# Optimization experiments

Hardware: AMD Instinct MI355X
Metric: run time of the kernel (lower is better)

The kernel has to match this reference:

```python
import jax, jax.numpy as jnp
import numpy as np
from jax import lax

DEPTH, HEADS, DH, DIM, M, V, NUM_EMB, D_VQ = 6, 8, 64, 512, 256, 523, 512, 64


def _ln(x, g, b):
    mu = jnp.mean(x, -1, keepdims=True)
    var = jnp.var(x, -1, keepdims=True)
    return (x - mu) * lax.rsqrt(var + 1e-5) * g + b


def _softmax_kernel(data, proj, is_query):
    # FAVOR+ positive softmax features (performer-pytorch softmax_kernel)
    dn = data * (data.shape[-1] ** -0.25)
    dd = jnp.einsum('bhld,md->bhlm', dn, proj)
    diag = 0.5 * jnp.sum(dn * dn, axis=-1, keepdims=True)
    mx = jnp.max(dd, axis=-1, keepdims=True) if is_query else jnp.max(dd)
    return jnp.exp(dd - diag - lax.stop_gradient(mx)) * (proj.shape[0] ** -0.5) + 1e-4


def _causal_linear_attn(qp, kp, v):
    # out_t = qp_t . cumsum_t(kp v^T) / (qp_t . cumsum_t(kp))
    kc = jnp.cumsum(kp, axis=2)
    den = jnp.einsum('bhlm,bhlm->bhl', qp, kc)
    kv = jnp.cumsum(jnp.einsum('bhlm,bhld->bhlmd', kp, v), axis=2)
    return jnp.einsum('bhlm,bhlmd->bhld', qp, kv) / den[..., None]


def _vq_encode(_x, conv1_w, conv1_b, conv2_w, conv2_b, codebook):
    dn = ('NCDHW', 'OIDHW', 'NCDHW')
    h = lax.conv_general_dilated(_x, conv1_w, (2, 2, 2), [(1, 1)] * 3, dimension_numbers=dn)
    h = jax.nn.relu(h + conv1_b[None, :, None, None, None])
    h = lax.conv_general_dilated(h, conv2_w, (2, 2, 2), [(1, 1)] * 3, dimension_numbers=dn)
    h = h + conv2_b[None, :, None, None, None]                 # [N, D, 4,4,4]
    z = jnp.transpose(h, (0, 2, 3, 4, 1))                      # [N, 4,4,4, D]
    flat = z.reshape(-1, z.shape[-1])
    d2 = (jnp.sum(flat * flat, 1, keepdims=True)
          - 2.0 * flat @ codebook.T
          + jnp.sum(codebook * codebook, 1)[None, :])
    inds = jnp.argmin(d2, axis=1).astype(jnp.int32)
    return inds.reshape(z.shape[:4])                           # [N, 4,4,4]


def _performer_loss(seq, tok_emb, pos_emb, proj, ln1_g, ln1_b, wq, wk, wv, wo, bo,
                    ln2_g, ln2_b, ff1_w, ff1_b, ff2_w, ff2_b, lnf_g, lnf_b,
                    logits_w, logits_b):
    inp, tgt = seq[:, :-1], seq[:, 1:]
    b, L = inp.shape
    h = tok_emb[inp] + pos_emb[:L][None]
    split = lambda t: jnp.transpose(t.reshape(b, L, HEADS, DH), (0, 2, 1, 3))
    for l in range(DEPTH):
        x1 = _ln(h, ln1_g[l], ln1_b[l])
        q, k, v = split(x1 @ wq[l]), split(x1 @ wk[l]), split(x1 @ wv[l])
        qp = _softmax_kernel(q, proj[l], True)
        kp = _softmax_kernel(k, proj[l], False)
        o = _causal_linear_attn(qp, kp, v)
        o = jnp.transpose(o, (0, 2, 1, 3)).reshape(b, L, DIM)
        h = h + o @ wo[l] + bo[l]
        x2 = _ln(h, ln2_g[l], ln2_b[l])
        h = h + jax.nn.gelu(x2 @ ff1_w[l] + ff1_b[l]) @ ff2_w[l] + ff2_b[l]
    h = _ln(h, lnf_g, lnf_b)
    logits = h @ logits_w + logits_b
    lp = jax.nn.log_softmax(logits, axis=-1)
    nll = -jnp.take_along_axis(lp, tgt[..., None], axis=-1)[..., 0]
    return jnp.mean(nll)


def setup_inputs() -> dict:
    key = jax.random.key(0)
    ks = jax.random.split(key, 24)
    n = lambda k, sh, s=0.02: (jax.random.normal(k, sh) * s).astype(jnp.float32)
    bs = 16
    return {
        'x': jax.random.normal(ks[0], (bs, 1, 16, 16, 16), jnp.float32),
        'xn': jax.random.normal(ks[1], (bs, 1, 1, 16, 16, 16), jnp.float32),
        'i': jax.random.randint(ks[2], (bs, 3), 0, V, jnp.int32),
        # frozen VQ-VAE
        'conv1_w': n(ks[3], (32, 1, 4, 4, 4), 0.1), 'conv1_b': jnp.zeros((32,), jnp.float32),
        'conv2_w': n(ks[4], (D_VQ, 32, 4, 4, 4), 0.05), 'conv2_b': jnp.zeros((D_VQ,), jnp.float32),
        'codebook': jax.random.normal(ks[5], (NUM_EMB, D_VQ), jnp.float32),
        # FAVOR+ random-feature projections (non-trainable buffer)
        'proj': jax.random.normal(ks[6], (DEPTH, M, DH), jnp.float32),
        # performer params
        'tok_emb': n(ks[7], (V, DIM)), 'pos_emb': n(ks[8], (131, DIM)),
        'ln1_g': jnp.ones((DEPTH, DIM), jnp.float32), 'ln1_b': jnp.zeros((DEPTH, DIM), jnp.float32),
        'wq': n(ks[9], (DEPTH, DIM, DIM)), 'wk': n(ks[10], (DEPTH, DIM, DIM)),
        'wv': n(ks[11], (DEPTH, DIM, DIM)), 'wo': n(ks[12], (DEPTH, DIM, DIM)),
        'bo': jnp.zeros((DEPTH, DIM), jnp.float32),
        'ln2_g': jnp.ones((DEPTH, DIM), jnp.float32), 'ln2_b': jnp.zeros((DEPTH, DIM), jnp.float32),
        'ff1_w': n(ks[13], (DEPTH, DIM, 4 * DIM)), 'ff1_b': jnp.zeros((DEPTH, 4 * DIM), jnp.float32),
        'ff2_w': n(ks[14], (DEPTH, 4 * DIM, DIM)), 'ff2_b': jnp.zeros((DEPTH, DIM), jnp.float32),
        'lnf_g': jnp.ones((DIM,), jnp.float32), 'lnf_b': jnp.zeros((DIM,), jnp.float32),
        'logits_w': n(ks[15], (DIM, V)), 'logits_b': jnp.zeros((V,), jnp.float32),
    }


def reference(x, xn, i, conv1_w, conv1_b, conv2_w, conv2_b, codebook, proj,
              tok_emb, pos_emb, ln1_g, ln1_b, wq, wk, wv, wo, bo, ln2_g, ln2_b,
              ff1_w, ff1_b, ff2_w, ff2_b, lnf_g, lnf_b, logits_w, logits_b):
    bs = x.shape[0]
    _xn = xn.reshape((-1,) + xn.shape[2:])            # (b n) c x y z
    _x = jnp.concatenate([x, _xn], axis=0)
    inds = _vq_encode(_x, conv1_w, conv1_b, conv2_w, conv2_b, codebook)
    inds_i = inds[:bs].reshape(bs, -1)                # b (x y z)
    inds_r = inds[bs:].reshape(bs, -1)                # b (n x y z)
    seq = jnp.concatenate([i.astype(jnp.int32), inds_r, inds_i], axis=1)  # [b, 131]
    return _performer_loss(seq, tok_emb, pos_emb, proj, ln1_g, ln1_b, wq, wk, wv, wo,
                           bo, ln2_g, ln2_b, ff1_w, ff1_b, ff2_w, ff2_b,
                           lnf_g, lnf_b, logits_w, logits_b)
```

## Files before the change

kernel.cpp:

```cpp
#include <hip/hip_runtime.h>

#define SEQL 130
#define LSEQ 131
#define DIMM 512
#define NHEADS 8
#define MF 256
#define VSZ 523
#define NROWS (16*SEQL)
#define NBH (16*NHEADS)
#define NBHL (NBH*SEQL)
#define QSEG 1064960
#define WLAYER 3145728

typedef __attribute__((ext_vector_type(8))) short short8;
typedef __attribute__((ext_vector_type(8))) unsigned short us8;
typedef __attribute__((ext_vector_type(4))) unsigned short us4;
typedef __attribute__((ext_vector_type(4))) float f32x4;

__device__ __forceinline__ unsigned short f2bf(float f){
  unsigned int u = __float_as_uint(f);
  u += 0x7fffu + ((u>>16)&1u);
  return (unsigned short)(u>>16);
}
__device__ __forceinline__ float bf2f(unsigned short h){
  return __uint_as_float(((unsigned int)h)<<16);
}
__device__ __forceinline__ float gelu_f(float x){
  float x3 = x*x*x;
  return 0.5f*x*(1.f+tanhf(0.7978845608028654f*(x+0.044715f*x3)));
}
__device__ __forceinline__ unsigned enc_max(float f){
  unsigned u = __float_as_uint(f);
  return (u & 0x80000000u) ? ~u : (u | 0x80000000u);
}
__device__ __forceinline__ float dec_max(unsigned k){
  unsigned u = (k>>31) ? (k & 0x7fffffffu) : ~k;
  return __uint_as_float(u);
}
__device__ __forceinline__ void gload16(const void* g, void* lds){
  __builtin_amdgcn_global_load_lds(
      (const __attribute__((address_space(1))) void*)g,
      (__attribute__((address_space(3))) void*)lds, 16, 0, 0);
}
__device__ __forceinline__ float blk_sum(float v){
  #pragma unroll
  for(int off=32;off;off>>=1) v += __shfl_xor(v,off);
  __shared__ float tmp_s[4];
  int t=threadIdx.x;
  if((t&63)==0) tmp_s[t>>6]=v;
  __syncthreads();
  v = tmp_s[0]+tmp_s[1]+tmp_s[2]+tmp_s[3];
  __syncthreads();
  return v;
}
__device__ __forceinline__ float blk_max(float v){
  #pragma unroll
  for(int off=32;off;off>>=1) v = fmaxf(v,__shfl_xor(v,off));
  __shared__ float tmp_m[4];
  int t=threadIdx.x;
  if((t&63)==0) tmp_m[t>>6]=v;
  __syncthreads();
  v = fmaxf(fmaxf(tmp_m[0],tmp_m[1]),fmaxf(tmp_m[2],tmp_m[3]));
  __syncthreads();
  return v;
}
__device__ __forceinline__ int tok_at(const int* __restrict__ iarr,
    const int* __restrict__ inds, int b, int p){
  if(p<3)  return iarr[b*3+p];
  if(p<67) return inds[(16+b)*64 + (p-3)];
  return inds[b*64 + (p-67)];
}

__global__ __launch_bounds__(256) void conv1_k(const float* __restrict__ x,
    const float* __restrict__ xn, const float* __restrict__ w,
    const float* __restrict__ bias, float* __restrict__ out){
  int idx = blockIdx.x*256 + threadIdx.x;
  if(idx >= 32*32*8*8*8) return;
  int ow = idx & 7, oh = (idx>>3)&7, od = (idx>>6)&7, oc = (idx>>9)&31, n = idx>>14;
  const float* xp = (n<16) ? (x + n*4096) : (xn + (n-16)*4096);
  const float* wp = w + oc*64;
  float acc = bias[oc];
  #pragma unroll
  for(int kd=0;kd<4;kd++){ int id = od*2-1+kd; if((unsigned)id>=16u) continue;
    #pragma unroll
    for(int kh=0;kh<4;kh++){ int ih = oh*2-1+kh; if((unsigned)ih>=16u) continue;
      #pragma unroll
      for(int kw=0;kw<4;kw++){ int iw = ow*2-1+kw; if((unsigned)iw>=16u) continue;
        acc += xp[(id*16+ih)*16+iw]*wp[(kd*4+kh)*4+kw];
      }}}
  out[idx] = fmaxf(acc,0.f);
}

__global__ __launch_bounds__(256) void cvt8_k(const float* __restrict__ src,
    unsigned short* __restrict__ dst, int n8){
  int i = blockIdx.x*256 + threadIdx.x;
  if(i >= n8) return;
  const float* s = src + (size_t)i*8;
  us8 u;
  #pragma unroll
  for(int j=0;j<8;j++) u[j] = f2bf(s[j]);
  *(us8*)(dst + (size_t)i*8) = u;
}

__global__ __launch_bounds__(256) void im2col_k(const float* __restrict__ c1,
    unsigned short* __restrict__ icol){
  int tid = blockIdx.x*256 + threadIdx.x;
  size_t e0 = (size_t)tid*8;
  int r = (int)(e0 >> 11);
  int k0 = (int)(e0 & 2047);
  int n = r>>6, od = (r>>4)&3, oh = (r>>2)&3, ow = r&3;
  int ic = k0>>6, kd = (k0>>4)&3, kh0 = (k0>>2)&3;
  int id = od*2 - 1 + kd;
  us8 u = {};
  if((unsigned)id < 8u){
    const float* base = c1 + (size_t)(n*32+ic)*512 + id*64;
    #pragma unroll
    for(int j=0;j<8;j++){
      int kh = kh0 + (j>>2), kw = j&3;
      int ih = oh*2 - 1 + kh, iw = ow*2 - 1 + kw;
      float v = 0.f;
      if((unsigned)ih < 8u && (unsigned)iw < 8u) v = base[ih*8 + iw];
      u[j] = f2bf(v);
    }
  }
  *(us8*)(icol + e0) = u;
}

__global__ __launch_bounds__(256) void vq_k(const float* __restrict__ z,
    const float* __restrict__ cb, int* __restrict__ inds){
  int nf = blockIdx.x;
  __shared__ float zs[64];
  int t = threadIdx.x;
  if(t<64) zs[t] = z[(size_t)nf*64 + t];
  __syncthreads();
  float best = 3.0e38f; int bi = 0;
  for(int j=t; j<512; j+=256){
    const float* cr = cb + j*64;
    float dot=0.f, nn=0.f;
    #pragma unroll 8
    for(int d=0;d<64;d++){ float cv=cr[d]; dot += zs[d]*cv; nn += cv*cv; }
    float dist = nn - 2.f*dot;
    if(dist < best){ best=dist; bi=j; }
  }
  #pragma unroll
  for(int off=32;off;off>>=1){
    float ob = __shfl_down(best,off); int oi = __shfl_down(bi,off);
    if(ob<best || (ob==best && oi<bi)){ best=ob; bi=oi; }
  }
  __shared__ float rb[4]; __shared__ int ri[4];
  if((t&63)==0){ rb[t>>6]=best; ri[t>>6]=bi; }
  __syncthreads();
  if(t==0){
    for(int wv=1;wv<4;wv++){ if(rb[wv]<best || (rb[wv]==best && ri[wv]<bi)){ best=rb[wv]; bi=ri[wv]; } }
    inds[nf]=bi;
  }
}

__global__ __launch_bounds__(256) void embed_k(const int* __restrict__ iarr,
    const int* __restrict__ inds, const float* __restrict__ tok,
    const float* __restrict__ pos, float* __restrict__ h){
  int idx = blockIdx.x*256 + threadIdx.x;
  int c = idx & 511; int row = idx >> 9;
  int b = row/SEQL, l = row - b*SEQL;
  int tk = tok_at(iarr, inds, b, l);
  h[idx] = tok[tk*DIMM + c] + pos[l*DIMM + c];
}

__global__ __launch_bounds__(256) void ln_k(const float* __restrict__ in,
    const float* __restrict__ g, const float* __restrict__ bb,
    unsigned short* __restrict__ out){
  int w = threadIdx.x>>6, l = threadIdx.x&63;
  int row = blockIdx.x*4 + w;
  const float* xr = in + (size_t)row*DIMM + l*8;
  f32x4 v0 = *(const f32x4*)xr;
  f32x4 v1 = *(const f32x4*)(xr+4);
  float s = v0[0]+v0[1]+v0[2]+v0[3]+v1[0]+v1[1]+v1[2]+v1[3];
  float ss = v0[0]*v0[0]+v0[1]*v0[1]+v0[2]*v0[2]+v0[3]*v0[3]
           + v1[0]*v1[0]+v1[1]*v1[1]+v1[2]*v1[2]+v1[3]*v1[3];
  #pragma unroll
  for(int off=32;off;off>>=1){ s += __shfl_xor(s,off); ss += __shfl_xor(ss,off); }
  float mu = s*(1.f/512.f);
  float var = ss*(1.f/512.f) - mu*mu;
  float inv = rsqrtf(var + 1e-5f);
  const float* gp = g + l*8; const float* bp = bb + l*8;
  us8 u;
  #pragma unroll
  for(int j=0;j<4;j++){
    u[j]   = f2bf((v0[j]-mu)*inv*gp[j]   + bp[j]);
    u[4+j] = f2bf((v1[j]-mu)*inv*gp[4+j] + bp[4+j]);
  }
  *(us8*)(out + (size_t)row*DIMM + l*8) = u;
}

__global__ __launch_bounds__(256) void wprep_k(const float* __restrict__ wq,
    const float* __restrict__ wk, const float* __restrict__ wv,
    const float* __restrict__ wo, const float* __restrict__ ff1,
    const float* __restrict__ ff2, unsigned short* __restrict__ wall,
    unsigned int* __restrict__ gmaxbits){
  int bid0 = blockIdx.x;
  int t = threadIdx.x;
  if(bid0==0 && t<8) gmaxbits[t] = 0u;
  int lyr = bid0 / 3072;
  int bid = bid0 - lyr*3072;
  unsigned short* wl = wall + (size_t)lyr*WLAYER;
  const float* src; unsigned short* dst;
  int n0, k0, srcN, dstK;
  if(bid < 768){
    int nt = bid % 48, kt = bid / 48;
    n0 = nt*32; k0 = kt*32;
    int seg = n0 >> 9;
    src = (seg==0 ? wq : seg==1 ? wk : wv) + (size_t)lyr*262144;
    dst = wl; srcN = 512; dstK = 512;
  } else if(bid < 1024){
    int b2 = bid-768; int nt = b2 % 16, kt = b2 / 16;
    n0 = nt*32; k0 = kt*32; src = wo + (size_t)lyr*262144;
    dst = wl + 786432; srcN = 512; dstK = 512;
  } else if(bid < 2048){
    int b2 = bid-1024; int nt = b2 % 64, kt = b2 / 64;
    n0 = nt*32; k0 = kt*32; src = ff1 + (size_t)lyr*1048576;
    dst = wl + 1048576; srcN = 2048; dstK = 512;
  } else {
    int b2 = bid-2048; int nt = b2 % 16, kt = b2 / 16;
    n0 = nt*32; k0 = kt*32; src = ff2 + (size_t)lyr*1048576;
    dst = wl + 2097152; srcN = 512; dstK = 2048;
  }
  int srcCol0 = (bid < 768) ? (n0 & 0x1ff) : n0;
  __shared__ float tile[32][33];
  int c = t&31, r = t>>5;
  #pragma unroll
  for(int j=0;j<4;j++)
    tile[r+8*j][c] = src[(size_t)(k0+r+8*j)*srcN + srcCol0 + c];
  __syncthreads();
  #pragma unroll
  for(int j=0;j<4;j++){
    int n = n0 + r + 8*j;
    dst[(size_t)n*dstK + k0 + c] = f2bf(tile[c][r+8*j]);
  }
}

__global__ __launch_bounds__(256) void wconv_k(const float* __restrict__ W,
    unsigned short* __restrict__ dst, int K, int N){
  __shared__ float tile[32][33];
  int k0 = blockIdx.y*32, n0 = blockIdx.x*32;
  int t = threadIdx.x; int c = t&31, r = t>>5;
  #pragma unroll
  for(int j=0;j<4;j++){
    int n = n0+c;
    tile[r+8*j][c] = (n<N) ? W[(size_t)(k0+r+8*j)*N + n] : 0.f;
  }
  __syncthreads();
  #pragma unroll
  for(int j=0;j<4;j++){
    int n = n0 + r + 8*j;
    if(n<N) dst[(size_t)n*K + k0 + c] = f2bf(tile[c][r+8*j]);
  }
}

template<int MODE>
__global__ __launch_bounds__(256) void gemm64x128_k(const unsigned short* __restrict__ A,
    const unsigned short* __restrict__ Bt, const float* __restrict__ bias,
    unsigned short* __restrict__ Cb, int M, int N, int K){
  __shared__ __attribute__((aligned(16))) unsigned short As[2][4096];
  __shared__ __attribute__((aligned(16))) unsigned short Bs[2][8192];
  int t = threadIdx.x, w = t>>6, l = t&63;
  const int m0 = blockIdx.y*64, n0 = blockIdx.x*128;
  int wr = w>>1, wc = w&1;
  f32x4 acc[2][4] = {};
  auto stage = [&](unsigned short* Ad, unsigned short* Bd, int k0){
    #pragma unroll
    for(int i=0;i<2;i++){
      int c = w*2 + i;
      int r = c*8 + (l>>3);
      int gc = k0 + (((l&7) ^ (r&7))<<3);
      int ar = m0 + r; if(ar >= M) ar = 0;
      gload16(A + (size_t)ar*K + gc, Ad + c*512);
    }
    #pragma unroll
    for(int i=0;i<4;i++){
      int c = w*4 + i;
      int r = c*8 + (l>>3);
      int gc = k0 + (((l&7) ^ (r&7))<<3);
      gload16(Bt + (size_t)(n0+r)*K + gc, Bd + c*512);
    }
  };
  stage(As[0], Bs[0], 0);
  int NTk = K>>6, buf = 0;
  for(int kt=0; kt<NTk; kt++){
    __syncthreads();
    if(kt+1 < NTk) stage(As[buf^1], Bs[buf^1], (kt+1)*64);
    const unsigned short* Ab = &As[buf][0];
    const unsigned short* Bb = &Bs[buf][0];
    #pragma unroll
    for(int kk=0;kk<2;kk++){
      short8 af[2], bf[4];
      #pragma unroll
      for(int m=0;m<2;m++){
        int row = wr*32 + m*16 + (l&15);
        int slot = kk*4 + (l>>4);
        af[m] = *(const short8*)(Ab + row*64 + ((slot^(row&7))<<3));
      }
      #pragma unroll
      for(int n=0;n<4;n++){
        int col = wc*64 + n*16 + (l&15);
        int slot = kk*4 + (l>>4);
        bf[n] = *(const short8*)(Bb + col*64 + ((slot^(col&7))<<3));
      }
      #pragma unroll
      for(int m=0;m<2;m++)
        #pragma unroll
        for(int n=0;n<4;n++)
          acc[m][n] = __builtin_amdgcn_mfma_f32_16x16x32_bf16(af[m], bf[n], acc[m][n], 0, 0, 0);
    }
    buf ^= 1;
  }
  #pragma unroll
  for(int m=0;m<2;m++){
    #pragma unroll
    for(int n=0;n<4;n++){
      int col = n0 + wc*64 + n*16 + (l&15);
      #pragma unroll
      for(int i=0;i<4;i++){
        int row = m0 + wr*32 + m*16 + (l>>4)*4 + i;
        if(row < M){
          float v = acc[m][n][i];
          if(MODE==1){
            v *= (col < 1024) ? 0.35355339059327378f : 1.0f;
            int seg = col>>9, d0 = col&511;
            int hh = d0>>6, d = d0&63;
            int bb = row/SEQL, ll = row - bb*SEQL;
            Cb[(size_t)seg*QSEG + (((size_t)(bb*NHEADS+hh))*SEQL + ll)*64 + d] = f2bf(v);
          } else {
            v += bias[col];
            v = gelu_f(v);
            Cb[(size_t)row*N+col] = f2bf(v);
          }
        }
      }
    }
  }
}

__global__ __launch_bounds__(256) void mgemm_k(const unsigned short* __restrict__ A,
    const unsigned short* __restrict__ Bt, const float* __restrict__ bias,
    float* __restrict__ Cf, int M, int N, int K){
  __shared__ __attribute__((aligned(16))) unsigned short As[2][4096];
  __shared__ __attribute__((aligned(16))) unsigned short Bs[2][4096];
  int t = threadIdx.x;
  const int m0 = blockIdx.y*64, n0 = blockIdx.x*64;
  int w = t>>6, l = t&63;
  int wr = w>>1, wc = w&1;
  f32x4 acc[2][2] = {};
  auto stage = [&](unsigned short* Ad, unsigned short* Bd, int k0){
    #pragma unroll
    for(int i=0;i<2;i++){
      int c = w*2 + i;
      int r = c*8 + (l>>3);
      int gc = k0 + (((l&7) ^ (r&7))<<3);
      int ar = m0 + r; if(ar >= M) ar = 0;
      gload16(A + (size_t)ar*K + gc, Ad + c*512);
      int br = n0 + r; if(br >= N) br = 0;
      gload16(Bt + (size_t)br*K + gc, Bd + c*512);
    }
  };
  stage(As[0], Bs[0], 0);
  int NT = K>>6;
  int buf = 0;
  for(int kt=0; kt<NT; kt++){
    __syncthreads();
    if(kt+1 < NT) stage(As[buf^1], Bs[buf^1], (kt+1)*64);
    const unsigned short* Ab = &As[buf][0];
    const unsigned short* Bb = &Bs[buf][0];
    #pragma unroll
    for(int kk=0;kk<2;kk++){
      short8 af[2], bf[2];
      #pragma unroll
      for(int m=0;m<2;m++){
        int row = wr*32 + m*16 + (l&15);
        int slot = kk*4 + (l>>4);
        af[m] = *(const short8*)(Ab + row*64 + ((slot^(row&7))<<3));
      }
      #pragma unroll
      for(int n=0;n<2;n++){
        int col = wc*32 + n*16 + (l&15);
        int slot = kk*4 + (l>>4);
        bf[n] = *(const short8*)(Bb + col*64 + ((slot^(col&7))<<3));
      }
      #pragma unroll
      for(int m=0;m<2;m++)
        #pragma unroll
        for(int n=0;n<2;n++)
          acc[m][n] = __builtin_amdgcn_mfma_f32_16x16x32_bf16(af[m], bf[n], acc[m][n], 0, 0, 0);
    }
    buf ^= 1;
  }
  #pragma unroll
  for(int m=0;m<2;m++){
    #pragma unroll
    for(int n=0;n<2;n++){
      int col = n0 + wc*32 + n*16 + (l&15);
      #pragma unroll
      for(int i=0;i<4;i++){
        int row = m0 + wr*32 + m*16 + (l>>4)*4 + i;
        if(row < M && col < N){
          Cf[(size_t)row*N+col] = acc[m][n][i] + bias[col];
        }
      }
    }
  }
}

template<int ACC>
__global__ __launch_bounds__(256) void mgemm32_k(const unsigned short* __restrict__ A,
    const unsigned short* __restrict__ Bt, const float* __restrict__ bias,
    float* __restrict__ Cf, int N, int K){
  __shared__ __attribute__((aligned(16))) unsigned short As[2][2048];
  __shared__ __attribute__((aligned(16))) unsigned short Bs[2][4096];
  int t = threadIdx.x;
  const int m0 = blockIdx.y*32, n0 = blockIdx.x*64;
  int w = t>>6, l = t&63;
  int wm = w&1, wn2 = w>>1;
  f32x4 acc[2] = {};
  auto stage = [&](unsigned short* Ad, unsigned short* Bd, int k0){
    {
      int c = w;
      int r = c*8 + (l>>3);
      int gc = k0 + (((l&7) ^ (r&7))<<3);
      gload16(A + (size_t)(m0+r)*K + gc, Ad + c*512);
    }
    #pragma unroll
    for(int i=0;i<2;i++){
      int c = w*2 + i;
      int r = c*8 + (l>>3);
      int gc = k0 + (((l&7) ^ (r&7))<<3);
      gload16(Bt + (size_t)(n0+r)*K + gc, Bd + c*512);
    }
  };
  stage(As[0], Bs[0], 0);
  int NT = K>>6;
  int buf = 0;
  for(int kt=0; kt<NT; kt++){
    __syncthreads();
    if(kt+1 < NT) stage(As[buf^1], Bs[buf^1], (kt+1)*64);
    const unsigned short* Ab = &As[buf][0];
    const unsigned short* Bb = &Bs[buf][0];
    #pragma unroll
    for(int kk=0;kk<2;kk++){
      int arow = wm*16 + (l&15);
      int slot = kk*4 + (l>>4);
      short8 af = *(const short8*)(Ab + arow*64 + ((slot^(arow&7))<<3));
      #pragma unroll
      for(int n=0;n<2;n++){
        int col = (wn2*2+n)*16 + (l&15);
        short8 bf = *(const short8*)(Bb + col*64 + ((slot^(col&7))<<3));
        acc[n] = __builtin_amdgcn_mfma_f32_16x16x32_bf16(af, bf, acc[n], 0, 0, 0);
      }
    }
    buf ^= 1;
  }
  #pragma unroll
  for(int n=0;n<2;n++){
    int col = n0 + (wn2*2+n)*16 + (l&15);
    float bv = bias[col];
    #pragma unroll
    for(int i=0;i<4;i++){
      int row = m0 + wm*16 + (l>>4)*4 + i;
      if(ACC) Cf[(size_t)row*N+col] += acc[n][i] + bv;
      else    Cf[(size_t)row*N+col]  = acc[n][i] + bv;
    }
  }
}

__global__ __launch_bounds__(256) void featA_k(const unsigned short* __restrict__ qn,
    const unsigned short* __restrict__ kn, const unsigned short* __restrict__ projl,
    unsigned short* __restrict__ qp, unsigned int* __restrict__ gmaxbits){
  int z = blockIdx.y;
  const unsigned short* dn = z ? kn : qn;
  __shared__ __attribute__((aligned(16))) float uni[32*264];
  __shared__ __attribute__((aligned(16))) unsigned short dns[2048];
  unsigned short* ps = (unsigned short*)uni;
  int t = threadIdx.x;
  int w = t>>6, l = t&63;
  size_t R0 = (size_t)blockIdx.x*32;
  {
    int c = w; int r = c*8 + (l>>3);
    int gc = (((l&7) ^ (r&7))<<3);
    gload16(dn + (R0+r)*64 + gc, dns + c*512);
  }
  #pragma unroll
  for(int i=0;i<8;i++){
    int c = w*8 + i; int r = c*8 + (l>>3);
    int gc = (((l&7) ^ (r&7))<<3);
    gload16(projl + (size_t)r*64 + gc, ps + c*512);
  }
  __syncthreads();
  int rt = w&1, cb = (w>>1)*8;
  f32x4 acc[8] = {};
  #pragma unroll
  for(int kk=0;kk<2;kk++){
    int ar = rt*16 + (l&15);
    int slot = kk*4 + (l>>4);
    short8 a = *(const short8*)(dns + ar*64 + ((slot^(ar&7))<<3));
    #pragma unroll
    for(int ct=0;ct<8;ct++){
      int br = (cb+ct)*16 + (l&15);
      short8 b = *(const short8*)(ps + br*64 + ((slot^(br&7))<<3));
      acc[ct] = __builtin_amdgcn_mfma_f32_16x16x32_bf16(a, b, acc[ct], 0, 0, 0);
    }
  }
  __syncthreads();
  #pragma unroll
  for(int ct=0;ct<8;ct++){
    int col = (cb+ct)*16 + (l&15);
    #pragma unroll
    for(int i=0;i<4;i++){
      int row = rt*16 + (l>>4)*4 + i;
      uni[row*264 + col] = acc[ct][i];
    }
  }
  __syncthreads();
  int r = t>>3, sub = t&7;
  float* rowp = uni + r*264 + sub*32;
  f32x4 v[8];
  #pragma unroll
  for(int jj=0;jj<8;jj++) v[jj] = *(const f32x4*)(rowp + jj*4);
  float m = -3.0e38f;
  #pragma unroll
  for(int jj=0;jj<8;jj++)
    #pragma unroll
    for(int i=0;i<4;i++) m = fmaxf(m, v[jj][i]);
  m = fmaxf(m, __shfl_xor(m,1));
  m = fmaxf(m, __shfl_xor(m,2));
  m = fmaxf(m, __shfl_xor(m,4));
  if(z==0){
    us8 dvu = *(const us8*)(dns + r*64 + ((sub^(r&7))<<3));
    float s2 = 0.f;
    #pragma unroll
    for(int j=0;j<8;j++){ float xx = bf2f(dvu[j]); s2 += xx*xx; }
    s2 += __shfl_xor(s2,1); s2 += __shfl_xor(s2,2); s2 += __shfl_xor(s2,4);
    float ds = 0.5f*s2;
    unsigned short* op = qp + (R0+r)*256 + sub*32;
    #pragma unroll
    for(int jj=0;jj<8;jj++){
      us4 u4;
      #pragma unroll
      for(int i=0;i<4;i++) u4[i] = f2bf(expf(v[jj][i] - ds - m)*0.0625f + 1e-4f);
      *(us4*)(op + jj*4) = u4;
    }
  } else {
    float bm = m;
    bm = fmaxf(bm, __shfl_xor(bm,8));
    bm = fmaxf(bm, __shfl_xor(bm,16));
    bm = fmaxf(bm, __shfl_xor(bm,32));
    __shared__ float wm[4];
    if(l==0) wm[w] = bm;
    __syncthreads();
    if(t==0){
      float g = fmaxf(fmaxf(wm[0],wm[1]),fmaxf(wm[2],wm[3]));
      atomicMax(gmaxbits, enc_max(g));
    }
  }
}

__global__ __launch_bounds__(256) void featB_k(const unsigned short* __restrict__ kn,
    const unsigned short* __restrict__ projl, const unsigned int* __restrict__ gmaxbits,
    unsigned short* __restrict__ kp){
  __shared__ __attribute__((aligned(16))) float uni[32*264];
  __shared__ __attribute__((aligned(16))) unsigned short dns[2048];
  unsigned short* ps = (unsigned short*)uni;
  int t = threadIdx.x;
  int w = t>>6, l = t&63;
  size_t R0 = (size_t)blockIdx.x*32;
  {
    int c = w; int r = c*8 + (l>>3);
    int gc = (((l&7) ^ (r&7))<<3);
    gload16(kn + (R0+r)*64 + gc, dns + c*512);
  }
  #pragma unroll
  for(int i=0;i<8;i++){
    int c = w*8 + i; int r = c*8 + (l>>3);
    int gc = (((l&7) ^ (r&7))<<3);
    gload16(projl + (size_t)r*64 + gc, ps + c*512);
  }
  __syncthreads();
  int rt = w&1, cb = (w>>1)*8;
  f32x4 acc[8] = {};
  #pragma unroll
  for(int kk=0;kk<2;kk++){
    int ar = rt*16 + (l&15);
    int slot = kk*4 + (l>>4);
    short8 a = *(const short8*)(dns + ar*64 + ((slot^(ar&7))<<3));
    #pragma unroll
    for(int ct=0;ct<8;ct++){
      int br = (cb+ct)*16 + (l&15);
      short8 b = *(const short8*)(ps + br*64 + ((slot^(br&7))<<3));
      acc[ct] = __builtin_amdgcn_mfma_f32_16x16x32_bf16(a, b, acc[ct], 0, 0, 0);
    }
  }
  __syncthreads();
  #pragma unroll
  for(int ct=0;ct<8;ct++){
    int col = (cb+ct)*16 + (l&15);
    #pragma unroll
    for(int i=0;i<4;i++){
      int row = rt*16 + (l>>4)*4 + i;
      uni[row*264 + col] = acc[ct][i];
    }
  }
  __syncthreads();
  float g = dec_max(gmaxbits[0]);
  int r = t>>3, sub = t&7;
  us8 dvu = *(const us8*)(dns + r*64 + ((sub^(r&7))<<3));
  float s2 = 0.f;
  #pragma unroll
  for(int j=0;j<8;j++){ float xx = bf2f(dvu[j]); s2 += xx*xx; }
  s2 += __shfl_xor(s2,1); s2 += __shfl_xor(s2,2); s2 += __shfl_xor(s2,4);
  float ds = 0.5f*s2;
  float* rowp = uni + r*264 + sub*32;
  unsigned short* op = kp + (R0+r)*256 + sub*32;
  #pragma unroll
  for(int jj=0;jj<8;jj++){
    f32x4 v = *(const f32x4*)(rowp + jj*4);
    us4 u4;
    #pragma unroll
    for(int i=0;i<4;i++) u4[i] = f2bf(expf(v[i] - ds - g)*0.0625f + 1e-4f);
    *(us4*)(op + jj*4) = u4;
  }
}

__global__ __launch_bounds__(256) void attn_k(const unsigned short* __restrict__ qp,
    const unsigned short* __restrict__ kp, const unsigned short* __restrict__ vn,
    unsigned short* __restrict__ ob){
  int qt = blockIdx.x, bh = blockIdx.y;
  int b = bh>>3, hh = bh&7;
  __shared__ __attribute__((aligned(16))) unsigned short qs[8192];
  __shared__ __attribute__((aligned(16))) unsigned short ks[8192];
  __shared__ __attribute__((aligned(16))) unsigned short VTs[64*34];
  __shared__ __attribute__((aligned(16))) unsigned short Sb[32*36];
  __shared__ float dens[2][32];
  int t = threadIdx.x;
  int w = t>>6, l = t&63;
  int qh = w>>1, nc = w&1;
  #pragma unroll
  for(int i=0;i<4;i++){
    int c = w*4 + i; int r = (c<<1) + (l>>5); int sl = l&31;
    int gc = ((sl ^ (r&7))<<3);
    int gr = qt*32 + r; if(gr >= SEQL) gr = 0;
    gload16(qp + ((size_t)bh*SEQL + gr)*256 + gc, qs + c*512);
  }
  if(t<64) dens[t>>5][t&31] = 0.f;
  f32x4 oacc[2] = {};
  for(int kt=0; kt<=qt; kt++){
    __syncthreads();
    #pragma unroll
    for(int i=0;i<4;i++){
      int c = w*4 + i; int r = (c<<1) + (l>>5); int sl = l&31;
      int gc = ((sl ^ (r&7))<<3);
      int gk = kt*32 + r; if(gk >= SEQL) gk = 0;
      gload16(kp + ((size_t)bh*SEQL + gk)*256 + gc, ks + c*512);
    }
    {
      int rr = t>>3, od = (t&7)*8;
      int gk = kt*32 + rr;
      us8 uv = {};
      if(gk < SEQL) uv = *(const us8*)(vn + ((size_t)bh*SEQL + gk)*64 + od);
      #pragma unroll
      for(int j=0;j<8;j++) VTs[(od+j)*34 + rr] = uv[j];
    }
    __syncthreads();
    f32x4 sacc = {};
    #pragma unroll
    for(int kk=0;kk<8;kk++){
      int ar = qh*16 + (l&15); int slot = kk*4 + (l>>4);
      short8 a = *(const short8*)(qs + ar*256 + ((slot^(ar&7))<<3));
      int br = nc*16 + (l&15);
      short8 bb2 = *(const short8*)(ks + br*256 + ((slot^(br&7))<<3));
      sacc = __builtin_amdgcn_mfma_f32_16x16x32_bf16(a, bb2, sacc, 0, 0, 0);
    }
    int scol = nc*16 + (l&15);
    int gcol = kt*32 + scol;
    float dp[4];
    #pragma unroll
    for(int i=0;i<4;i++){
      int sr = qh*16 + (l>>4)*4 + i;
      int grw = qt*32 + sr;
      float v2 = sacc[i];
      if(gcol > grw) v2 = 0.f;
      Sb[sr*36 + scol] = f2bf(v2);
      dp[i] = v2;
    }
    #pragma unroll
    for(int off=1;off<16;off<<=1)
      #pragma unroll
      for(int i=0;i<4;i++) dp[i] += __shfl_xor(dp[i], off);
    if((l&15)==0){
      #pragma unroll
      for(int i=0;i<4;i++) dens[nc][qh*16 + (l>>4)*4 + i] += dp[i];
    }
    __syncthreads();
    short8 a2 = *(const short8*)(Sb + (qh*16 + (l&15))*36 + (l>>4)*8);
    #pragma unroll
    for(int n2=0;n2<2;n2++){
      int d = nc*32 + n2*16 + (l&15);
      short8 b2 = *(const short8*)(VTs + d*34 + (l>>4)*8);
      oacc[n2] = __builtin_amdgcn_mfma_f32_16x16x32_bf16(a2, b2, oacc[n2], 0, 0, 0);
    }
  }
  __syncthreads();
  #pragma unroll
  for(int n2=0;n2<2;n2++){
    int d = nc*32 + n2*16 + (l&15);
    #pragma unroll
    for(int i=0;i<4;i++){
      int rit = qh*16 + (l>>4)*4 + i;
      int gr = qt*32 + rit;
      if(gr < SEQL){
        float inv = 1.f/(dens[0][rit] + dens[1][rit]);
        ob[((size_t)(b*SEQL+gr))*DIMM + hh*64 + d] = f2bf(oacc[n2][i]*inv);
      }
    }
  }
}

__global__ __launch_bounds__(256) void loss_k(const float* __restrict__ logits,
    const int* __restrict__ iarr, const int* __restrict__ inds,
    float* __restrict__ rnll){
  int row = blockIdx.x; int t = threadIdx.x;
  const float* lr = logits + (size_t)row*VSZ;
  float m = -3.0e38f;
  for(int j=t;j<VSZ;j+=256) m = fmaxf(m, lr[j]);
  m = blk_max(m);
  float s = 0.f;
  for(int j=t;j<VSZ;j+=256) s += expf(lr[j]-m);
  s = blk_sum(s);
  if(t==0){
    int b = row/SEQL, l = row - b*SEQL;
    int tgt = tok_at(iarr, inds, b, l+1);
    rnll[row] = (m + logf(s)) - lr[tgt];
  }
}

__global__ __launch_bounds__(256) void fin_k(const float* __restrict__ rnll,
    float* __restrict__ out){
  int t = threadIdx.x;
  float s = 0.f;
  for(int i=t;i<NROWS;i+=256) s += rnll[i];
  s = blk_sum(s);
  if(t==0) out[0] = s/(float)NROWS;
}

extern "C" void kernel_launch(void* const* d_in, const int* in_sizes, int n_in,
                              void* d_out, int out_size, void* d_ws, size_t ws_size,
                              hipStream_t stream){
  (void)in_sizes; (void)n_in; (void)out_size; (void)ws_size;
  const float* x        = (const float*)d_in[0];
  const float* xn       = (const float*)d_in[1];
  const int*   iarr     = (const int*)  d_in[2];
  const float* conv1_w  = (const float*)d_in[3];
  const float* conv1_b  = (const float*)d_in[4];
  const float* conv2_w  = (const float*)d_in[5];
  const float* conv2_b  = (const float*)d_in[6];
  const float* codebook = (const float*)d_in[7];
  const float* proj     = (const float*)d_in[8];
  const float* tok_emb  = (const float*)d_in[9];
  const float* pos_emb  = (const float*)d_in[10];
  const float* ln1_g    = (const float*)d_in[11];
  const float* ln1_b    = (const float*)d_in[12];
  const float* wq       = (const float*)d_in[13];
  const float* wk       = (const float*)d_in[14];
  const float* wv       = (const float*)d_in[15];
  const float* wo       = (const float*)d_in[16];
  const float* bo       = (const float*)d_in[17];
  const float* ln2_g    = (const float*)d_in[18];
  const float* ln2_b    = (const float*)d_in[19];
  const float* ff1_w    = (const float*)d_in[20];
  const float* ff1_b    = (const float*)d_in[21];
  const float* ff2_w    = (const float*)d_in[22];
  const float* ff2_b    = (const float*)d_in[23];
  const float* lnf_g    = (const float*)d_in[24];
  const float* lnf_b    = (const float*)d_in[25];
  const float* logits_w = (const float*)d_in[26];
  const float* logits_b = (const float*)d_in[27];

  float* wsf = (float*)d_ws;
  size_t off = 0;
  unsigned short* qp_bf = (unsigned short*)(wsf + off); off += 2129920;
  unsigned short* kp_bf = (unsigned short*)(wsf + off); off += 2129920;
  float* h = wsf + off; off += 1064960;
  unsigned short* x1b = (unsigned short*)(wsf + off); off += 532480;
  unsigned short* qkvb = (unsigned short*)(wsf + off); off += 1597440;
  unsigned short* ob  = (unsigned short*)(wsf + off); off += 532480;
  unsigned short* projb = (unsigned short*)(wsf + off); off += 49152;
  unsigned short* wall  = (unsigned short*)(wsf + off); off += 9437184;
  unsigned short* logt  = (unsigned short*)(wsf + off); off += 133888;
  unsigned short* ffmid = (unsigned short*)(wsf + off); off += 2129920;
  float* logits = wsf + off; off += 1087840;
  int* inds = (int*)(wsf + off); off += 2048;
  unsigned int* gmaxbits = (unsigned int*)(wsf + off); off += 64;
  float* rnll = wsf + off; off += 2112;

  float* c1 = logits;
  unsigned short* icol = ffmid;
  float* zbuf = (float*)qp_bf;
  unsigned short* cw2b = (unsigned short*)kp_bf;

  unsigned short* qnb = qkvb;
  unsigned short* knb = qkvb + QSEG;
  unsigned short* vnb = qkvb + 2*QSEG;

  conv1_k<<<2048,256,0,stream>>>(x, xn, conv1_w, conv1_b, c1);
  cvt8_k<<<64,256,0,stream>>>(conv2_w, cw2b, 16384);
  im2col_k<<<2048,256,0,stream>>>(c1, icol);
  mgemm32_k<0><<<dim3(1,64),256,0,stream>>>(icol, cw2b, conv2_b, zbuf, 64, 2048);
  vq_k<<<2048,256,0,stream>>>(zbuf, codebook, inds);
  embed_k<<<(NROWS*DIMM)/256,256,0,stream>>>(iarr, inds, tok_emb, pos_emb, h);
  cvt8_k<<<48,256,0,stream>>>(proj, projb, 12288);
  wconv_k<<<dim3(17,16),256,0,stream>>>(logits_w, logt, 512, 523);
  wprep_k<<<18432,256,0,stream>>>(wq, wk, wv, wo, ff1_w, ff2_w, wall, gmaxbits);

  for(int l=0;l<6;l++){
    unsigned short* wl    = wall + (size_t)l*WLAYER;
    unsigned short* wqkvt = wl;
    unsigned short* wot   = wl + 786432;
    unsigned short* ff1t  = wl + 1048576;
    unsigned short* ff2t  = wl + 2097152;
    ln_k<<<520,256,0,stream>>>(h, ln1_g+l*DIMM, ln1_b+l*DIMM, x1b);
    gemm64x128_k<1><<<dim3(12,33),256,0,stream>>>(x1b, wqkvt, nullptr, qkvb, NROWS, 1536, DIMM);
    featA_k<<<dim3(520,2),256,0,stream>>>(qnb, knb, projb + l*16384, qp_bf, gmaxbits + l);
    featB_k<<<520,256,0,stream>>>(knb, projb + l*16384, gmaxbits + l, kp_bf);
    attn_k<<<dim3(5,NBH),256,0,stream>>>(qp_bf, kp_bf, vnb, ob);
    mgemm32_k<1><<<dim3(8,65),256,0,stream>>>(ob, wot, bo+l*DIMM, h, DIMM, DIMM);
    ln_k<<<520,256,0,stream>>>(h, ln2_g+l*DIMM, ln2_b+l*DIMM, x1b);
    gemm64x128_k<4><<<dim3(16,33),256,0,stream>>>(x1b, ff1t, ff1_b+l*2048, ffmid, NROWS, 2048, DIMM);
    mgemm32_k<1><<<dim3(8,65),256,0,stream>>>(ffmid, ff2t, ff2_b+l*DIMM, h, DIMM, 2048);
  }

  ln_k<<<520,256,0,stream>>>(h, lnf_g, lnf_b, x1b);
  mgemm_k<<<dim3(9,33),256,0,stream>>>(x1b, logt, logits_b, logits, NROWS, VSZ, DIMM);
  loss_k<<<NROWS,256,0,stream>>>(logits, iarr, inds, rnll);
  fin_k<<<1,256,0,stream>>>(rnll, (float*)d_out);
}
```

Measured before the change: 735.1 us.

## Merge weight-prep kernels, restructure attention staging, retile FF2 GEMM

Folds the separate bf16 conversion and transpose kernels (conv2, proj, logits weights) into one prep launch, which cuts launch overhead. The attention kernel now loads all key/value tiles into LDS up front and runs its score and output phases without a barrier per tile, at the cost of much larger LDS use and lower occupancy. The FF2 projection switches from the 32-row residual GEMM to a 64x64 tile mgemm variant that accumulates into h, halving the grid rows.

```diff
diff --git a/kernel.cpp b/kernel.cpp
--- a/kernel.cpp
+++ b/kernel.cpp
@@ -89,17 +89,6 @@
         acc += xp[(id*16+ih)*16+iw]*wp[(kd*4+kh)*4+kw];
       }}}
   out[idx] = fmaxf(acc,0.f);
-}
-
-__global__ __launch_bounds__(256) void cvt8_k(const float* __restrict__ src,
-    unsigned short* __restrict__ dst, int n8){
-  int i = blockIdx.x*256 + threadIdx.x;
-  if(i >= n8) return;
-  const float* s = src + (size_t)i*8;
-  us8 u;
-  #pragma unroll
-  for(int j=0;j<8;j++) u[j] = f2bf(s[j]);
-  *(us8*)(dst + (size_t)i*8) = u;
 }
 
 __global__ __launch_bounds__(256) void im2col_k(const float* __restrict__ c1,
@@ -192,67 +181,84 @@
   *(us8*)(out + (size_t)row*DIMM + l*8) = u;
 }
 
-__global__ __launch_bounds__(256) void wprep_k(const float* __restrict__ wq,
+__global__ __launch_bounds__(256) void prep_k(const float* __restrict__ wq,
     const float* __restrict__ wk, const float* __restrict__ wv,
     const float* __restrict__ wo, const float* __restrict__ ff1,
     const float* __restrict__ ff2, unsigned short* __restrict__ wall,
+    const float* __restrict__ conv2_w, unsigned short* __restrict__ cw2b,
+    const float* __restrict__ proj, unsigned short* __restrict__ projb,
+    const float* __restrict__ logits_w, unsigned short* __restrict__ logt,
     unsigned int* __restrict__ gmaxbits){
   int bid0 = blockIdx.x;
   int t = threadIdx.x;
   if(bid0==0 && t<8) gmaxbits[t] = 0u;
-  int lyr = bid0 / 3072;
-  int bid = bid0 - lyr*3072;
-  unsigned short* wl = wall + (size_t)lyr*WLAYER;
-  const float* src; unsigned short* dst;
-  int n0, k0, srcN, dstK;
-  if(bid < 768){
-    int nt = bid % 48, kt = bid / 48;
-    n0 = nt*32; k0 = kt*32;
-    int seg = n0 >> 9;
-    src = (seg==0 ? wq : seg==1 ? wk : wv) + (size_t)lyr*262144;
-    dst = wl; srcN = 512; dstK = 512;
-  } else if(bid < 1024){
-    int b2 = bid-768; int nt = b2 % 16, kt = b2 / 16;
-    n0 = nt*32; k0 = kt*32; src = wo + (size_t)lyr*262144;
-    dst = wl + 786432; srcN = 512; dstK = 512;
-  } else if(bid < 2048){
-    int b2 = bid-1024; int nt = b2 % 64, kt = b2 / 64;
-    n0 = nt*32; k0 = kt*32; src = ff1 + (size_t)lyr*1048576;
-    dst = wl + 1048576; srcN = 2048; dstK = 512;
-  } else {
-    int b2 = bid-2048; int nt = b2 % 16, kt = b2 / 16;
-    n0 = nt*32; k0 = kt*32; src = ff2 + (size_t)lyr*1048576;
-    dst = wl + 2097152; srcN = 512; dstK = 2048;
-  }
-  int srcCol0 = (bid < 768) ? (n0 & 0x1ff) : n0;
-  __shared__ float tile[32][33];
-  int c = t&31, r = t>>5;
-  #pragma unroll
-  for(int j=0;j<4;j++)
-    tile[r+8*j][c] = src[(size_t)(k0+r+8*j)*srcN + srcCol0 + c];
-  __syncthreads();
-  #pragma unroll
-  for(int j=0;j<4;j++){
-    int n = n0 + r + 8*j;
-    dst[(size_t)n*dstK + k0 + c] = f2bf(tile[c][r+8*j]);
-  }
-}
-
-__global__ __launch_bounds__(256) void wconv_k(const float* __restrict__ W,
-    unsigned short* __restrict__ dst, int K, int N){
-  __shared__ float tile[32][33];
-  int k0 = blockIdx.y*32, n0 = blockIdx.x*32;
-  int t = threadIdx.x; int c = t&31, r = t>>5;
-  #pragma unroll
-  for(int j=0;j<4;j++){
-    int n = n0+c;
-    tile[r+8*j][c] = (n<N) ? W[(size_t)(k0+r+8*j)*N + n] : 0.f;
-  }
-  __syncthreads();
-  #pragma unroll
-  for(int j=0;j<4;j++){
-    int n = n0 + r + 8*j;
-    if(n<N) dst[(size_t)n*K + k0 + c] = f2bf(tile[c][r+8*j]);
+  if(bid0 < 18432){
+    int lyr = bid0 / 3072;
+    int bid = bid0 - lyr*3072;
+    unsigned short* wl = wall + (size_t)lyr*WLAYER;
+    const float* src; unsigned short* dst;
+    int n0, k0, srcN, dstK;
+    if(bid < 768){
+      int nt = bid % 48, kt = bid / 48;
+      n0 = nt*32; k0 = kt*32;
+      int seg = n0 >> 9;
+      src = (seg==0 ? wq : seg==1 ? wk : wv) + (size_t)lyr*262144;
+      dst = wl; srcN = 512; dstK = 512;
+    } else if(bid < 1024){
+      int b2 = bid-768; int nt = b2 % 16, kt = b2 / 16;
+      n0 = nt*32; k0 = kt*32; src = wo + (size_t)lyr*262144;
+      dst = wl + 786432; srcN = 512; dstK = 512;
+    } else if(bid < 2048){
+      int b2 = bid-1024; int nt = b2 % 64, kt = b2 / 64;
+      n0 = nt*32; k0 = kt*32; src = ff1 + (size_t)lyr*1048576;
+      dst = wl + 1048576; srcN = 2048; dstK = 512;
+    } else {
+      int b2 = bid-2048; int nt = b2 % 16, kt = b2 / 16;
+      n0 = nt*32; k0 = kt*32; src = ff2 + (size_t)lyr*1048576;
+      dst = wl + 2097152; srcN = 512; dstK = 2048;
+    }
+    int srcCol0 = (bid < 768) ? (n0 & 0x1ff) : n0;
+    __shared__ float tile[32][33];
+    int c = t&31, r = t>>5;
+    #pragma unroll
+    for(int j=0;j<4;j++)
+      tile[r+8*j][c] = src[(size_t)(k0+r+8*j)*srcN + srcCol0 + c];
+    __syncthreads();
+    #pragma unroll
+    for(int j=0;j<4;j++){
+      int n = n0 + r + 8*j;
+      dst[(size_t)n*dstK + k0 + c] = f2bf(tile[c][r+8*j]);
+    }
+    return;
+  }
+  if(bid0 < 18544){
+    const float* src; unsigned short* dst; int i;
+    if(bid0 < 18496){ i = (bid0-18432)*256 + t; src = conv2_w; dst = cw2b; }
+    else            { i = (bid0-18496)*256 + t; src = proj;    dst = projb; }
+    const float* s = src + (size_t)i*8;
+    us8 u;
+    #pragma unroll
+    for(int j=0;j<8;j++) u[j] = f2bf(s[j]);
+    *(us8*)(dst + (size_t)i*8) = u;
+    return;
+  }
+  {
+    int b2 = bid0 - 18544;
+    int nt = b2 % 17, kt = b2 / 17;
+    int n0 = nt*32, k0 = kt*32;
+    __shared__ float tile[32][33];
+    int c = t&31, r = t>>5;
+    #pragma unroll
+    for(int j=0;j<4;j++){
+      int n = n0+c;
+      tile[r+8*j][c] = (n<VSZ) ? logits_w[(size_t)(k0+r+8*j)*VSZ + n] : 0.f;
+    }
+    __syncthreads();
+    #pragma unroll
+    for(int j=0;j<4;j++){
+      int n = n0 + r + 8*j;
+      if(n<VSZ) logt[(size_t)n*512 + k0 + c] = f2bf(tile[c][r+8*j]);
+    }
   }
 }
 
@@ -340,6 +346,7 @@
   }
 }
 
+template<int MODE>
 __global__ __launch_bounds__(256) void mgemm_k(const unsigned short* __restrict__ A,
     const unsigned short* __restrict__ Bt, const float* __restrict__ bias,
     float* __restrict__ Cf, int M, int N, int K){
@@ -402,7 +409,8 @@
       for(int i=0;i<4;i++){
         int row = m0 + wr*32 + m*16 + (l>>4)*4 + i;
         if(row < M && col < N){
-          Cf[(size_t)row*N+col] = acc[m][n][i] + bias[col];
+          if(MODE==3) Cf[(size_t)row*N+col] += acc[m][n][i] + bias[col];
+          else        Cf[(size_t)row*N+col]  = acc[m][n][i] + bias[col];
         }
       }
     }
@@ -633,9 +641,9 @@
   int qt = blockIdx.x, bh = blockIdx.y;
   int b = bh>>3, hh = bh&7;
   __shared__ __attribute__((aligned(16))) unsigned short qs[8192];
-  __shared__ __attribute__((aligned(16))) unsigned short ks[8192];
-  __shared__ __attribute__((aligned(16))) unsigned short VTs[64*34];
-  __shared__ __attribute__((aligned(16))) unsigned short Sb[32*36];
+  __shared__ __attribute__((aligned(16))) unsigned short ks[5*8192];
+  __shared__ __attribute__((aligned(16))) unsigned short VTs[5*2176];
+  __shared__ __attribute__((aligned(16))) unsigned short Sb[5*1152];
   __shared__ float dens[2][32];
   int t = threadIdx.x;
   int w = t>>6, l = t&63;
@@ -647,16 +655,13 @@
     int gr = qt*32 + r; if(gr >= SEQL) gr = 0;
     gload16(qp + ((size_t)bh*SEQL + gr)*256 + gc, qs + c*512);
   }
-  if(t<64) dens[t>>5][t&31] = 0.f;
-  f32x4 oacc[2] = {};
   for(int kt=0; kt<=qt; kt++){
-    __syncthreads();
     #pragma unroll
     for(int i=0;i<4;i++){
       int c = w*4 + i; int r = (c<<1) + (l>>5); int sl = l&31;
       int gc = ((sl ^ (r&7))<<3);
       int gk = kt*32 + r; if(gk >= SEQL) gk = 0;
-      gload16(kp + ((size_t)bh*SEQL + gk)*256 + gc, ks + c*512);
+      gload16(kp + ((size_t)bh*SEQL + gk)*256 + gc, ks + kt*8192 + c*512);
     }
     {
       int rr = t>>3, od = (t&7)*8;
@@ -664,16 +669,20 @@
       us8 uv = {};
       if(gk < SEQL) uv = *(const us8*)(vn + ((size_t)bh*SEQL + gk)*64 + od);
       #pragma unroll
-      for(int j=0;j<8;j++) VTs[(od+j)*34 + rr] = uv[j];
-    }
-    __syncthreads();
+      for(int j=0;j<8;j++) VTs[kt*2176 + (od+j)*34 + rr] = uv[j];
+    }
+  }
+  __syncthreads();
+  float dreg[4] = {0.f,0.f,0.f,0.f};
+  for(int kt=0; kt<=qt; kt++){
+    const unsigned short* kb = ks + kt*8192;
     f32x4 sacc = {};
     #pragma unroll
     for(int kk=0;kk<8;kk++){
       int ar = qh*16 + (l&15); int slot = kk*4 + (l>>4);
       short8 a = *(const short8*)(qs + ar*256 + ((slot^(ar&7))<<3));
       int br = nc*16 + (l&15);
-      short8 bb2 = *(const short8*)(ks + br*256 + ((slot^(br&7))<<3));
+      short8 bb2 = *(const short8*)(kb + br*256 + ((slot^(br&7))<<3));
       sacc = __builtin_amdgcn_mfma_f32_16x16x32_bf16(a, bb2, sacc, 0, 0, 0);
     }
     int scol = nc*16 + (l&15);
@@ -685,27 +694,31 @@
       int grw = qt*32 + sr;
       float v2 = sacc[i];
       if(gcol > grw) v2 = 0.f;
-      Sb[sr*36 + scol] = f2bf(v2);
+      Sb[kt*1152 + sr*36 + scol] = f2bf(v2);
       dp[i] = v2;
     }
     #pragma unroll
     for(int off=1;off<16;off<<=1)
       #pragma unroll
       for(int i=0;i<4;i++) dp[i] += __shfl_xor(dp[i], off);
-    if((l&15)==0){
-      #pragma unroll
-      for(int i=0;i<4;i++) dens[nc][qh*16 + (l>>4)*4 + i] += dp[i];
-    }
-    __syncthreads();
-    short8 a2 = *(const short8*)(Sb + (qh*16 + (l&15))*36 + (l>>4)*8);
+    #pragma unroll
+    for(int i=0;i<4;i++) dreg[i] += dp[i];
+  }
+  if((l&15)==0){
+    #pragma unroll
+    for(int i=0;i<4;i++) dens[nc][qh*16 + (l>>4)*4 + i] = dreg[i];
+  }
+  __syncthreads();
+  f32x4 oacc[2] = {};
+  for(int kt=0; kt<=qt; kt++){
+    short8 a2 = *(const short8*)(Sb + kt*1152 + (qh*16 + (l&15))*36 + (l>>4)*8);
     #pragma unroll
     for(int n2=0;n2<2;n2++){
       int d = nc*32 + n2*16 + (l&15);
-      short8 b2 = *(const short8*)(VTs + d*34 + (l>>4)*8);
+      short8 b2 = *(const short8*)(VTs + kt*2176 + d*34 + (l>>4)*8);
       oacc[n2] = __builtin_amdgcn_mfma_f32_16x16x32_bf16(a2, b2, oacc[n2], 0, 0, 0);
     }
   }
-  __syncthreads();
   #pragma unroll
   for(int n2=0;n2<2;n2++){
     int d = nc*32 + n2*16 + (l&15);
@@ -807,15 +820,13 @@
   unsigned short* knb = qkvb + QSEG;
   unsigned short* vnb = qkvb + 2*QSEG;
 
+  prep_k<<<18816,256,0,stream>>>(wq, wk, wv, wo, ff1_w, ff2_w, wall,
+      conv2_w, cw2b, proj, projb, logits_w, logt, gmaxbits);
   conv1_k<<<2048,256,0,stream>>>(x, xn, conv1_w, conv1_b, c1);
-  cvt8_k<<<64,256,0,stream>>>(conv2_w, cw2b, 16384);
   im2col_k<<<2048,256,0,stream>>>(c1, icol);
   mgemm32_k<0><<<dim3(1,64),256,0,stream>>>(icol, cw2b, conv2_b, zbuf, 64, 2048);
   vq_k<<<2048,256,0,stream>>>(zbuf, codebook, inds);
   embed_k<<<(NROWS*DIMM)/256,256,0,stream>>>(iarr, inds, tok_emb, pos_emb, h);
-  cvt8_k<<<48,256,0,stream>>>(proj, projb, 12288);
-  wconv_k<<<dim3(17,16),256,0,stream>>>(logits_w, logt, 512, 523);
-  wprep_k<<<18432,256,0,stream>>>(wq, wk, wv, wo, ff1_w, ff2_w, wall, gmaxbits);
 
   for(int l=0;l<6;l++){
     unsigned short* wl    = wall + (size_t)l*WLAYER;
@@ -831,11 +842,11 @@
     mgemm32_k<1><<<dim3(8,65),256,0,stream>>>(ob, wot, bo+l*DIMM, h, DIMM, DIMM);
     ln_k<<<520,256,0,stream>>>(h, ln2_g+l*DIMM, ln2_b+l*DIMM, x1b);
     gemm64x128_k<4><<<dim3(16,33),256,0,stream>>>(x1b, ff1t, ff1_b+l*2048, ffmid, NROWS, 2048, DIMM);
-    mgemm32_k<1><<<dim3(8,65),256,0,stream>>>(ffmid, ff2t, ff2_b+l*DIMM, h, DIMM, 2048);
+    mgemm_k<3><<<dim3(8,33),256,0,stream>>>(ffmid, ff2t, ff2_b+l*DIMM, h, NROWS, DIMM, 2048);
   }
 
   ln_k<<<520,256,0,stream>>>(h, lnf_g, lnf_b, x1b);
-  mgemm_k<<<dim3(9,33),256,0,stream>>>(x1b, logt, logits_b, logits, NROWS, VSZ, DIMM);
+  mgemm_k<0><<<dim3(9,33),256,0,stream>>>(x1b, logt, logits_b, logits, NROWS, VSZ, DIMM);
   loss_k<<<NROWS,256,0,stream>>>(logits, iarr, inds, rnll);
   fin_k<<<1,256,0,stream>>>(rnll, (float*)d_out);
 }
```

New measurement: 781.4 us. 1.06x slower.
